# Performance work log

Hardware: AMD Instinct MI355X
Metric: run time of the kernel (lower is better)

The kernel has to match this reference:

```python
import jax, jax.numpy as jnp
import numpy as np

B, LAT, H, D, T = 2048, 32, 256, 20, 512  # batch, latent, hidden, output, max_len


def setup_inputs() -> dict:
    key = jax.random.key(0)
    ks = jax.random.split(key, 16)
    s = 0.05  # weight scale
    n = lambda k, shape, sc=s: jax.random.normal(k, shape, dtype=jnp.float32) * sc
    return {
        "z": n(ks[0], (B, LAT), 1.0),
        "target_lengths": jax.random.randint(ks[1], (B,), 1, T + 1),
        "max_len": T,
        # latent -> initial hidden / cell (hidden_dim * num_layers outputs)
        "w_lh": n(ks[2], (2 * H, LAT)), "b_lh": n(ks[3], (2 * H,)),
        "w_lc": n(ks[4], (2 * H, LAT)), "b_lc": n(ks[5], (2 * H,)),
        # LSTM layer 0 (input = output_dim), gates ordered i,f,g,o (PyTorch)
        "w_ih0": n(ks[6], (4 * H, D)), "w_hh0": n(ks[7], (4 * H, H)),
        "b_ih0": n(ks[8], (4 * H,)), "b_hh0": n(ks[9], (4 * H,)),
        # LSTM layer 1 (input = hidden_dim)
        "w_ih1": n(ks[10], (4 * H, H)), "w_hh1": n(ks[11], (4 * H, H)),
        "b_ih1": n(ks[12], (4 * H,)), "b_hh1": n(ks[13], (4 * H,)),
        # output projection
        "w_proj": n(ks[14], (D, H)), "b_proj": n(ks[15], (D,)),
    }


def _lstm_cell(x, h, c, w_ih, w_hh, b_ih, b_hh):
    g = x @ w_ih.T + b_ih + h @ w_hh.T + b_hh  # [B, 4H]
    i, f, gg, o = jnp.split(g, 4, axis=-1)
    c = jax.nn.sigmoid(f) * c + jax.nn.sigmoid(i) * jnp.tanh(gg)
    h = jax.nn.sigmoid(o) * jnp.tanh(c)
    return h, c


def reference(z, target_lengths, max_len,
              w_lh, b_lh, w_lc, b_lc,
              w_ih0, w_hh0, b_ih0, b_hh0,
              w_ih1, w_hh1, b_ih1, b_hh1,
              w_proj, b_proj):
    batch = z.shape[0]
    hid = w_hh0.shape[1]
    out_dim = w_ih0.shape[1]
    # initial per-layer states: view(B, num_layers, H)
    h_init = (z @ w_lh.T + b_lh).reshape(batch, 2, hid)
    c_init = (z @ w_lc.T + b_lc).reshape(batch, 2, hid)
    h0, h1 = h_init[:, 0], h_init[:, 1]
    c0, c1 = c_init[:, 0], c_init[:, 1]
    x0 = jnp.zeros((batch, out_dim), dtype=z.dtype)

    def step(carry, _):
        x, h0, c0, h1, c1 = carry
        h0, c0 = _lstm_cell(x, h0, c0, w_ih0, w_hh0, b_ih0, b_hh0)
        h1, c1 = _lstm_cell(h0, h1, c1, w_ih1, w_hh1, b_ih1, b_hh1)
        y = h1 @ w_proj.T + b_proj  # [B, D], fed back as next input
        return (y, h0, c0, h1, c1), y

    _, ys = jax.lax.scan(step, (x0, h0, c0, h1, c1), None, length=int(max_len))
    return jnp.transpose(ys, (1, 0, 2))  # [B, T, D]
```

## Files before the change

kernel.cpp:

```cpp
#include <hip/hip_runtime.h>
#include <hip/hip_bf16.h>

#define NB 32
#define TT 512
#define DD 20

using bf16x8 = __attribute__((ext_vector_type(8))) short;
using f32x4  = __attribute__((ext_vector_type(4))) float;

typedef __attribute__((address_space(3))) unsigned int lds_uint;
typedef __attribute__((address_space(1))) unsigned int glob_uint;

#define OFF_WSTR  0
#define OFF_WPROJ 1638400
#define OFF_B0    1654784
#define OFF_B1    1658880
#define OFF_EXCH  1662976
#define OFF_FLAG  3760128
#define WS_NEED_QUAD 3762176
#define WQUARTER  409600
#define WSTR_BYTES 1638400

#define QM_H0    0
#define QM_H1    16896
#define QM_XB    33792
#define QM_WPS   35840
#define QM_ZB    52224
#define QM_RING  56320
#define QM_TOTAL 121856

#define SM_RING  0
#define SM_H0    98304
#define SM_H1    115200
#define SM_XB    132096
#define SM_WPS   134144
#define SM_ZB    150528
#define SM_TOTAL 154624

__device__ __forceinline__ float sigf(float x) { return 1.0f / (1.0f + __expf(-x)); }
__device__ __forceinline__ float tanhfast(float x) { return 1.0f - 2.0f / (__expf(2.0f * x) + 1.0f); }

__device__ __forceinline__ void stage16(const char* g, const char* l) {
    __builtin_amdgcn_global_load_lds((glob_uint*)g, (lds_uint*)l, 16, 0, 0);
}

#define BARRIER_LK do { \
    asm volatile("s_waitcnt lgkmcnt(0)" ::: "memory"); \
    __builtin_amdgcn_s_barrier(); \
    asm volatile("" ::: "memory"); \
    __builtin_amdgcn_sched_barrier(0); \
} while (0)

__global__ void prep_quad(const float* __restrict__ wih0, const float* __restrict__ whh0,
                          const float* __restrict__ wih1, const float* __restrict__ whh1,
                          const float* __restrict__ wproj,
                          const float* __restrict__ bih0, const float* __restrict__ bhh0,
                          const float* __restrict__ bih1, const float* __restrict__ bhh1,
                          char* __restrict__ ws) {
    int idx = blockIdx.x * 256 + threadIdx.x;
    if (idx < 819200) {
        int g  = idx / 204800;
        int r  = idx - g * 204800;
        int u  = r >> 13;
        int r2 = r & 8191;
        int w  = r2 >> 11;
        int r3 = r2 & 2047;
        int q  = r3 >> 9;
        int e2 = r3 & 511;
        const float* src; int K, kt;
        if (u < 8)       { src = whh0; K = 256; kt = u; }
        else if (u == 8) { src = wih0; K = 20;  kt = 0; }
        else if (u < 17) { src = whh1; K = 256; kt = u - 9; }
        else             { src = wih1; K = 256; kt = u - 17; }
        int NT = q * 16 + g * 4 + w;
        int j = e2 & 7, lane = e2 >> 3;
        int n = NT * 16 + (lane & 15);
        int k = kt * 32 + ((lane >> 4) << 3) + j;
        float v = (k < K) ? src[n * K + k] : 0.0f;
        ((__hip_bfloat16*)(ws + OFF_WSTR))[idx] = __float2bfloat16(v);
    } else if (idx < 827392) {
        int e = idx - 819200;
        int j = e & 7, lane = (e >> 3) & 63, tile = e >> 9;
        int kt = tile & 7, nt = tile >> 3;
        int n = nt * 16 + (lane & 15);
        int k = kt * 32 + ((lane >> 4) << 3) + j;
        float v = (n < 20) ? wproj[n * 256 + k] : 0.0f;
        ((__hip_bfloat16*)(ws + OFF_WPROJ))[e] = __float2bfloat16(v);
    } else if (idx < 828416) {
        int j = idx - 827392; ((float*)(ws + OFF_B0))[j] = bih0[j] + bhh0[j];
    } else if (idx < 829440) {
        int j = idx - 828416; ((float*)(ws + OFF_B1))[j] = bih1[j] + bhh1[j];
    } else if (idx < 829952) {
        ((unsigned int*)(ws + OFF_FLAG))[idx - 829440] = 0;
    }
}

__global__ __launch_bounds__(256, 1) void decoder_quad(
    const float* __restrict__ z, const float* __restrict__ w_lh, const float* __restrict__ b_lh,
    const float* __restrict__ w_lc, const float* __restrict__ b_lc,
    const float* __restrict__ b_proj, char* __restrict__ ws,
    float* __restrict__ out) {

    __shared__ __align__(16) char smem[QM_TOTAL];

    const int tid = threadIdx.x;
    const int grp = blockIdx.x & 63;
    const int g   = blockIdx.x >> 6;
    const int b0  = grp * NB;

    __hip_bfloat16* h0p = (__hip_bfloat16*)(smem + QM_H0);
    __hip_bfloat16* h1p = (__hip_bfloat16*)(smem + QM_H1);
    __hip_bfloat16* xbh = (__hip_bfloat16*)(smem + QM_XB);

    {
        float* zbf = (float*)(smem + QM_ZB);
        #pragma unroll
        for (int i = 0; i < 4; i++) {
            int ii = tid + i * 256;
            zbf[ii] = z[(b0 + (ii >> 5)) * 32 + (ii & 31)];
        }
        ((unsigned int*)(smem + QM_XB))[tid]       = 0;
        ((unsigned int*)(smem + QM_XB))[tid + 256] = 0;
        const bf16x8* sp = (const bf16x8*)(ws + OFF_WPROJ);
        bf16x8* dp = (bf16x8*)(smem + QM_WPS);
        #pragma unroll
        for (int i = 0; i < 4; i++) dp[tid + i * 256] = sp[tid + i * 256];
    }
    __syncthreads();

    {
        float* cinitf = (float*)(smem + QM_RING);
        const float* zbf = (const float*)(smem + QM_ZB);
        for (int ii = 0; ii < 64; ii++) {
            int pi = ii * 256 + tid;
            int b = pi >> 9, col = pi & 511;
            float dh = b_lh[col], dc = b_lc[col];
            #pragma unroll 8
            for (int k = 0; k < 32; k++) {
                float zv = zbf[b * 32 + k];
                dh += zv * w_lh[col * 32 + k];
                dc += zv * w_lc[col * 32 + k];
            }
            if (col < 256) { h0p[b * 264 + col]         = __float2bfloat16(dh); cinitf[b * 256 + col]                 = dc; }
            else           { h1p[b * 264 + (col - 256)] = __float2bfloat16(dh); cinitf[8192 + b * 256 + (col - 256)] = dc; }
        }
    }
    __syncthreads();

    const int w  = tid >> 6, ln = tid & 63;
    const int l15 = ln & 15, lq = ln >> 4;
    const int lnoff = ln * 16;
    const int colg = g * 64 + w * 16 + l15;

    float c0r[2][4], c1r[2][4];
    {
        const float* cinitf = (const float*)(smem + QM_RING);
        #pragma unroll
        for (int mt = 0; mt < 2; mt++)
            #pragma unroll
            for (int r = 0; r < 4; r++) {
                int m = mt * 16 + lq * 4 + r;
                c0r[mt][r] = cinitf[m * 256 + colg];
                c1r[mt][r] = cinitf[8192 + m * 256 + colg];
            }
    }
    __syncthreads();

    const float* bias0 = (const float*)(ws + OFF_B0);
    const float* bias1 = (const float*)(ws + OFF_B1);
    float bs0[4], bs1[4];
    #pragma unroll
    for (int q = 0; q < 4; q++) {
        bs0[q] = bias0[q * 256 + colg];
        bs1[q] = bias1[q * 256 + colg];
    }
    const int pc_nt = w & 1, pc_mt = w >> 1;
    const int pc_col = pc_nt * 16 + l15;
    const float bpj = (pc_col < 20) ? b_proj[pc_col] : 0.0f;

    const char* wps_c = smem + QM_WPS;
    const char* h0c = smem + QM_H0;
    const char* h1c = smem + QM_H1;
    const char* xbc = smem + QM_XB;
    float* outp = out;

    const char* wgl   = ws + OFF_WSTR + g * WQUARTER + w * 4096 + lnoff;
    char*       ringb = smem + QM_RING + w * 16384;
    const char* ringc = smem + QM_RING + w * 16384 + lnoff;
    int sOff = 0;
    int slS  = 0;
    int slR  = 0;

    f32x4 acc[4][2];
    bf16x8 wT0, wT1, wT2, wT3, afA, afB;

#define STAGE_NEXT do { \
    stage16(wgl + sOff,        ringb + slS * 4096); \
    stage16(wgl + sOff + 1024, ringb + slS * 4096 + 1024); \
    stage16(wgl + sOff + 2048, ringb + slS * 4096 + 2048); \
    stage16(wgl + sOff + 3072, ringb + slS * 4096 + 3072); \
    sOff += 16384; if (sOff >= WQUARTER) sOff = 0; \
    slS = (slS + 1) & 3; \
} while (0)

#define WWAIT do { \
    asm volatile("s_waitcnt vmcnt(8)" ::: "memory"); \
    __builtin_amdgcn_sched_barrier(0); \
} while (0)

#define LOADW do { \
    const char* rb_ = ringc + slR * 4096; slR = (slR + 1) & 3; \
    wT0 = *(const bf16x8*)(rb_); \
    wT1 = *(const bf16x8*)(rb_ + 1024); \
    wT2 = *(const bf16x8*)(rb_ + 2048); \
    wT3 = *(const bf16x8*)(rb_ + 3072); \
} while (0)

#define LOADA(hsrc, ktv) do { \
    afA = *(const bf16x8*)((hsrc) + l15 * 528 + (ktv) * 64 + lq * 16); \
    afB = *(const bf16x8*)((hsrc) + (16 + l15) * 528 + (ktv) * 64 + lq * 16); \
} while (0)

#define LOADAX do { \
    afA = *(const bf16x8*)(xbc + l15 * 64 + lq * 16); \
    afB = *(const bf16x8*)(xbc + (16 + l15) * 64 + lq * 16); \
} while (0)

#define MFMA8 do { \
    acc[0][0] = __builtin_amdgcn_mfma_f32_16x16x32_bf16(afA, wT0, acc[0][0], 0, 0, 0); \
    acc[0][1] = __builtin_amdgcn_mfma_f32_16x16x32_bf16(afB, wT0, acc[0][1], 0, 0, 0); \
    acc[1][0] = __builtin_amdgcn_mfma_f32_16x16x32_bf16(afA, wT1, acc[1][0], 0, 0, 0); \
    acc[1][1] = __builtin_amdgcn_mfma_f32_16x16x32_bf16(afB, wT1, acc[1][1], 0, 0, 0); \
    acc[2][0] = __builtin_amdgcn_mfma_f32_16x16x32_bf16(afA, wT2, acc[2][0], 0, 0, 0); \
    acc[2][1] = __builtin_amdgcn_mfma_f32_16x16x32_bf16(afB, wT2, acc[2][1], 0, 0, 0); \
    acc[3][0] = __builtin_amdgcn_mfma_f32_16x16x32_bf16(afA, wT3, acc[3][0], 0, 0, 0); \
    acc[3][1] = __builtin_amdgcn_mfma_f32_16x16x32_bf16(afB, wT3, acc[3][1], 0, 0, 0); \
} while (0)

    auto phaseC = [&](int t) {
        f32x4 py = {bpj, bpj, bpj, bpj};
        #pragma unroll
        for (int kt = 0; kt < 8; kt++) {
            bf16x8 ah = *(const bf16x8*)(h1c + (pc_mt * 16 + l15) * 528 + kt * 64 + lq * 16);
            bf16x8 wf = *(const bf16x8*)(wps_c + pc_nt * 8192 + kt * 1024 + lnoff);
            py = __builtin_amdgcn_mfma_f32_16x16x32_bf16(ah, wf, py, 0, 0, 0);
        }
        if (pc_col < 20) {
            #pragma unroll
            for (int r = 0; r < 4; r++) {
                int row = pc_mt * 16 + lq * 4 + r;
                if (g == 0)
                    outp[((size_t)(b0 + row) * TT + (t - 1)) * DD + pc_col] = py[r];
                xbh[row * 32 + pc_col] = __float2bfloat16(py[r]);
            }
        }
    };

    unsigned int* exBase = (unsigned int*)(ws + OFF_EXCH);
    unsigned int* flBase = (unsigned int*)(ws + OFF_FLAG);

    auto exchStore = [&](int L, const char* hp, int t) {
        unsigned int* exO = exBase + ((grp * 2 + L) * 4 + g) * 1024;
        unsigned int* flO = flBase + (grp * 2 + L) * 4 + g;
        #pragma unroll
        for (int i = 0; i < 4; i++) {
            int wi = tid * 4 + i, m = wi >> 5, cp = wi & 31;
            unsigned int v = *(const unsigned int*)(hp + m * 528 + g * 128 + cp * 4);
            __hip_atomic_store(&exO[wi], v, __ATOMIC_RELAXED, __HIP_MEMORY_SCOPE_AGENT);
        }
        asm volatile("s_waitcnt vmcnt(0)" ::: "memory");
        if (tid == 0)
            __hip_atomic_store(flO, (unsigned int)(t + 1), __ATOMIC_RELAXED, __HIP_MEMORY_SCOPE_AGENT);
    };

    auto exchFinish = [&](int L, char* hp, unsigned int expect) {
        if (tid < 3) {
            int p = tid + (tid >= g);
            unsigned int* flP = flBase + (grp * 2 + L) * 4 + p;
            int spins = 0;
            while (__hip_atomic_load(flP, __ATOMIC_RELAXED, __HIP_MEMORY_SCOPE_AGENT) < expect) {
                __builtin_amdgcn_s_sleep(8);
                if (++spins > (1 << 11)) break;
            }
        }
        BARRIER_LK;
        #pragma unroll
        for (int pp = 0; pp < 3; pp++) {
            int p = pp + (pp >= g);
            unsigned int* exP = exBase + ((grp * 2 + L) * 4 + p) * 1024;
            unsigned int pv[4];
            #pragma unroll
            for (int i = 0; i < 4; i++)
                pv[i] = __hip_atomic_load(&exP[tid * 4 + i], __ATOMIC_RELAXED, __HIP_MEMORY_SCOPE_AGENT);
            #pragma unroll
            for (int i = 0; i < 4; i++) {
                int wi = tid * 4 + i, m = wi >> 5, cp = wi & 31;
                *(unsigned int*)(hp + m * 528 + p * 128 + cp * 4) = pv[i];
            }
        }
        BARRIER_LK;
    };

    STAGE_NEXT;
    STAGE_NEXT;
    STAGE_NEXT;
    WWAIT;
    LOADW;
    LOADA(h0c, 0);

    #pragma unroll 1
    for (int t = 0; t < TT; t++) {
        #pragma unroll
        for (int q = 0; q < 4; q++) {
            f32x4 v = {bs0[q], bs0[q], bs0[q], bs0[q]};
            acc[q][0] = v; acc[q][1] = v;
        }
        #pragma unroll 1
        for (int kt = 0; kt < 7; kt++) {
            STAGE_NEXT; MFMA8; WWAIT; LOADW; LOADA(h0c, kt + 1);
        }
        if (t > 0) {
            exchFinish(1, (char*)(smem + QM_H1), (unsigned int)t);
            phaseC(t);
        }
        BARRIER_LK;
        STAGE_NEXT; MFMA8; WWAIT; LOADW; LOADAX;
        STAGE_NEXT; MFMA8; WWAIT; LOADW; LOADA(h1c, 0);
        BARRIER_LK;

        #pragma unroll
        for (int mt = 0; mt < 2; mt++)
            #pragma unroll
            for (int r = 0; r < 4; r++) {
                float iv = acc[0][mt][r], fv = acc[1][mt][r];
                float gv = acc[2][mt][r], ov = acc[3][mt][r];
                float cn = sigf(fv) * c0r[mt][r] + sigf(iv) * tanhfast(gv);
                float hn = sigf(ov) * tanhfast(cn);
                c0r[mt][r] = cn;
                h0p[(mt * 16 + lq * 4 + r) * 264 + colg] = __float2bfloat16(hn);
            }
        BARRIER_LK;
        exchStore(0, h0c, t);

        #pragma unroll
        for (int q = 0; q < 4; q++) {
            f32x4 v = {bs1[q], bs1[q], bs1[q], bs1[q]};
            acc[q][0] = v; acc[q][1] = v;
        }
        #pragma unroll 1
        for (int kt = 0; kt < 7; kt++) {
            STAGE_NEXT; MFMA8; WWAIT; LOADW; LOADA(h1c, kt + 1);
        }
        STAGE_NEXT; MFMA8; WWAIT; LOADW;
        exchFinish(0, (char*)(smem + QM_H0), (unsigned int)(t + 1));
        LOADA(h0c, 0);
        #pragma unroll 1
        for (int kt = 0; kt < 7; kt++) {
            STAGE_NEXT; MFMA8; WWAIT; LOADW; LOADA(h0c, kt + 1);
        }
        STAGE_NEXT; MFMA8; WWAIT; LOADW; LOADA(h0c, 0);
        BARRIER_LK;

        #pragma unroll
        for (int mt = 0; mt < 2; mt++)
            #pragma unroll
            for (int r = 0; r < 4; r++) {
                float iv = acc[0][mt][r], fv = acc[1][mt][r];
                float gv = acc[2][mt][r], ov = acc[3][mt][r];
                float cn = sigf(fv) * c1r[mt][r] + sigf(iv) * tanhfast(gv);
                float hn = sigf(ov) * tanhfast(cn);
                c1r[mt][r] = cn;
                h1p[(mt * 16 + lq * 4 + r) * 264 + colg] = __float2bfloat16(hn);
            }
        BARRIER_LK;
        exchStore(1, h1c, t);
    }

    exchFinish(1, (char*)(smem + QM_H1), (unsigned int)TT);
    phaseC(TT);

#undef STAGE_NEXT
#undef WWAIT
#undef LOADW
#undef LOADA
#undef LOADAX
#undef MFMA8
}


__global__ void prep_solo(const float* __restrict__ wih0, const float* __restrict__ whh0,
                          const float* __restrict__ wih1, const float* __restrict__ whh1,
                          const float* __restrict__ wproj,
                          const float* __restrict__ bih0, const float* __restrict__ bhh0,
                          const float* __restrict__ bih1, const float* __restrict__ bhh1,
                          char* __restrict__ ws) {
    int idx = blockIdx.x * 256 + threadIdx.x;
    if (idx < 819200) {
        int s  = idx >> 12;
        int wv = (idx >> 9) & 7;
        int e2 = idx & 511;
        int u = s >> 2, qq = s & 3, half = u & 1;
        const float* src; int K, kt;
        if (u < 16)      { src = whh0; K = 256; kt = u >> 1; }
        else if (u < 18) { src = wih0; K = 20;  kt = 0; }
        else if (u < 34) { src = wih1; K = 256; kt = (u - 18) >> 1; }
        else             { src = whh1; K = 256; kt = (u - 34) >> 1; }
        int NT = half * 32 + (qq >> 1) * 16 + wv * 2 + (qq & 1);
        int j = e2 & 7, lane = e2 >> 3;
        int n = NT * 16 + (lane & 15);
        int k = kt * 32 + ((lane >> 4) << 3) + j;
        float v = (k < K) ? src[n * K + k] : 0.0f;
        ((__hip_bfloat16*)(ws + OFF_WSTR))[idx] = __float2bfloat16(v);
    } else if (idx < 827392) {
        int e = idx - 819200;
        int j = e & 7, lane = (e >> 3) & 63, tile = e >> 9;
        int kt = tile & 7, nt = tile >> 3;
        int n = nt * 16 + (lane & 15);
        int k = kt * 32 + ((lane >> 4) << 3) + j;
        float v = (n < 20) ? wproj[n * 256 + k] : 0.0f;
        ((__hip_bfloat16*)(ws + OFF_WPROJ))[e] = __float2bfloat16(v);
    } else if (idx < 828416) {
        int j = idx - 827392; ((float*)(ws + OFF_B0))[j] = bih0[j] + bhh0[j];
    } else if (idx < 829440) {
        int j = idx - 828416; ((float*)(ws + OFF_B1))[j] = bih1[j] + bhh1[j];
    }
}

__global__ __launch_bounds__(512, 1) void decoder_solo(
    const float* __restrict__ z, const float* __restrict__ w_lh, const float* __restrict__ b_lh,
    const float* __restrict__ w_lc, const float* __restrict__ b_lc,
    const float* __restrict__ b_proj, const char* __restrict__ ws,
    float* __restrict__ out) {

    __shared__ __align__(16) char smem[SM_TOTAL];

    const int tid = threadIdx.x;
    const int b0  = blockIdx.x * NB;

    __hip_bfloat16* h0p = (__hip_bfloat16*)(smem + SM_H0);
    __hip_bfloat16* h1p = (__hip_bfloat16*)(smem + SM_H1);
    __hip_bfloat16* xbh = (__hip_bfloat16*)(smem + SM_XB);

    {
        float* zbf = (float*)(smem + SM_ZB);
        zbf[tid]       = z[(b0 + (tid >> 5)) * 32 + (tid & 31)];
        int i2 = tid + 512;
        zbf[i2]        = z[(b0 + (i2 >> 5)) * 32 + (i2 & 31)];
        ((unsigned int*)(smem + SM_XB))[tid] = 0;
        const bf16x8* sp = (const bf16x8*)(ws + OFF_WPROJ);
        bf16x8* dp = (bf16x8*)(smem + SM_WPS);
        dp[tid] = sp[tid];
        dp[tid + 512] = sp[tid + 512];
    }
    __syncthreads();

    {
        float* cinitf = (float*)smem;
        const float* zbf = (const float*)(smem + SM_ZB);
        for (int ii = 0; ii < 32; ii++) {
            int pi = ii * 512 + tid;
            int b = pi >> 9, col = pi & 511;
            float dh = b_lh[col], dc = b_lc[col];
            #pragma unroll 8
            for (int k = 0; k < 32; k++) {
                float zv = zbf[b * 32 + k];
                dh += zv * w_lh[col * 32 + k];
                dc += zv * w_lc[col * 32 + k];
            }
            if (col < 256) { h0p[b * 264 + col]         = __float2bfloat16(dh); cinitf[b * 256 + col]                 = dc; }
            else           { h1p[b * 264 + (col - 256)] = __float2bfloat16(dh); cinitf[8192 + b * 256 + (col - 256)] = dc; }
        }
    }
    __syncthreads();

    const int wv = tid >> 6, ln = tid & 63;
    const int l15 = ln & 15, lq = ln >> 4;
    const int lnoff = ln * 16;

    float c0r[2][2][4], c1r[2][2][4];
    {
        const float* cinitf = (const float*)smem;
        #pragma unroll
        for (int mt = 0; mt < 2; mt++)
            #pragma unroll
            for (int h = 0; h < 2; h++)
                #pragma unroll
                for (int r = 0; r < 4; r++) {
                    int m = mt * 16 + lq * 4 + r, u = wv * 32 + h * 16 + l15;
                    c0r[mt][h][r] = cinitf[m * 256 + u];
                    c1r[mt][h][r] = cinitf[8192 + m * 256 + u];
                }
    }
    __syncthreads();

    const float* bias0 = (const float*)(ws + OFF_B0);
    const float* bias1 = (const float*)(ws + OFF_B1);
    float bs0[8], bs1[8];
    #pragma unroll
    for (int q = 0; q < 8; q++) {
        int col = (q >> 1) * 256 + wv * 32 + (q & 1) * 16 + l15;
        bs0[q] = bias0[col];
        bs1[q] = bias1[col];
    }
    const int pc_nt = wv & 1, pc_mt = wv >> 1;
    const int pc_col = pc_nt * 16 + l15;
    const float bpj = (wv < 4 && pc_col < 20) ? b_proj[pc_col] : 0.0f;

    const char* wps_c = smem + SM_WPS;
    const char* h0c = smem + SM_H0;
    const char* h1c = smem + SM_H1;
    const char* xbc = smem + SM_XB;

    float* outp = out;

    const char* wgl   = ws + OFF_WSTR + wv * 1024 + lnoff;
    char*       ringb = smem + SM_RING + wv * 12288;
    const char* ringc = smem + SM_RING + wv * 12288 + lnoff;
    int sOff = 2 * 32768;
    int slS  = 2;
    int slR  = 0;

    f32x4 acc[8][2];

    auto doPanel = [&](const char* hsrc, int kt, bool isX, int qbase) {
        bf16x8 af0, af1;
        if (isX) {
            af0 = *(const bf16x8*)(xbc + l15 * 64 + lq * 16);
            af1 = *(const bf16x8*)(xbc + (16 + l15) * 64 + lq * 16);
        } else {
            af0 = *(const bf16x8*)(hsrc + l15 * 528 + kt * 64 + lq * 16);
            af1 = *(const bf16x8*)(hsrc + (16 + l15) * 528 + kt * 64 + lq * 16);
        }
        #pragma unroll
        for (int j = 0; j < 4; j++)
            stage16(wgl + (sOff + j * 8192), ringb + slS * 4096 + j * 1024);
        sOff += 32768; if (sOff >= WSTR_BYTES) sOff = 0;
        slS = (slS == 2) ? 0 : slS + 1;
        asm volatile("s_waitcnt vmcnt(8)" ::: "memory");
        __builtin_amdgcn_sched_barrier(0);
        const char* rb = ringc + slR * 4096;
        slR = (slR == 2) ? 0 : slR + 1;
        bf16x8 w0 = *(const bf16x8*)(rb);
        bf16x8 w1 = *(const bf16x8*)(rb + 1024);
        bf16x8 w2 = *(const bf16x8*)(rb + 2048);
        bf16x8 w3 = *(const bf16x8*)(rb + 3072);
        acc[qbase + 0][0] = __builtin_amdgcn_mfma_f32_16x16x32_bf16(af0, w0, acc[qbase + 0][0], 0, 0, 0);
        acc[qbase + 0][1] = __builtin_amdgcn_mfma_f32_16x16x32_bf16(af1, w0, acc[qbase + 0][1], 0, 0, 0);
        acc[qbase + 1][0] = __builtin_amdgcn_mfma_f32_16x16x32_bf16(af0, w1, acc[qbase + 1][0], 0, 0, 0);
        acc[qbase + 1][1] = __builtin_amdgcn_mfma_f32_16x16x32_bf16(af1, w1, acc[qbase + 1][1], 0, 0, 0);
        acc[qbase + 2][0] = __builtin_amdgcn_mfma_f32_16x16x32_bf16(af0, w2, acc[qbase + 2][0], 0, 0, 0);
        acc[qbase + 2][1] = __builtin_amdgcn_mfma_f32_16x16x32_bf16(af1, w2, acc[qbase + 2][1], 0, 0, 0);
        acc[qbase + 3][0] = __builtin_amdgcn_mfma_f32_16x16x32_bf16(af0, w3, acc[qbase + 3][0], 0, 0, 0);
        acc[qbase + 3][1] = __builtin_amdgcn_mfma_f32_16x16x32_bf16(af1, w3, acc[qbase + 3][1], 0, 0, 0);
    };

    auto phaseC = [&](int t) {
        f32x4 py = {bpj, bpj, bpj, bpj};
        #pragma unroll
        for (int kt = 0; kt < 8; kt++) {
            bf16x8 ah = *(const bf16x8*)(h1c + (pc_mt * 16 + l15) * 528 + kt * 64 + lq * 16);
            bf16x8 wf = *(const bf16x8*)(wps_c + pc_nt * 8192 + kt * 1024 + lnoff);
            py = __builtin_amdgcn_mfma_f32_16x16x32_bf16(ah, wf, py, 0, 0, 0);
        }
        if (pc_col < 20) {
            #pragma unroll
            for (int r = 0; r < 4; r++) {
                int row = pc_mt * 16 + lq * 4 + r;
                outp[((size_t)(b0 + row) * TT + (t - 1)) * DD + pc_col] = py[r];
                xbh[row * 32 + pc_col] = __float2bfloat16(py[r]);
            }
        }
    };

    #pragma unroll
    for (int j = 0; j < 4; j++) stage16(wgl + j * 8192,         ringb + j * 1024);
    #pragma unroll
    for (int j = 0; j < 4; j++) stage16(wgl + 32768 + j * 8192, ringb + 4096 + j * 1024);

    #pragma unroll 1
    for (int t = 0; t < TT; t++) {
        #pragma unroll
        for (int q = 0; q < 8; q++) {
            f32x4 v = {bs0[q], bs0[q], bs0[q], bs0[q]};
            acc[q][0] = v; acc[q][1] = v;
        }
        if (t > 0 && wv < 4) phaseC(t);
        #pragma unroll 1
        for (int uu = 0; uu < 7; uu++) {
            doPanel(h0c, uu, false, 0);
            doPanel(h0c, uu, false, 4);
        }
        BARRIER_LK;
        doPanel(h0c, 7, false, 0);
        doPanel(h0c, 7, false, 4);
        doPanel(xbc, 0, true,  0);
        doPanel(xbc, 0, true,  4);
        BARRIER_LK;

        #pragma unroll
        for (int mt = 0; mt < 2; mt++)
            #pragma unroll
            for (int h = 0; h < 2; h++)
                #pragma unroll
                for (int r = 0; r < 4; r++) {
                    float iv = acc[0 + h][mt][r], fv = acc[2 + h][mt][r];
                    float gv = acc[4 + h][mt][r], ov = acc[6 + h][mt][r];
                    float cn = sigf(fv) * c0r[mt][h][r] + sigf(iv) * tanhfast(gv);
                    float hn = sigf(ov) * tanhfast(cn);
                    c0r[mt][h][r] = cn;
                    h0p[(mt * 16 + lq * 4 + r) * 264 + wv * 32 + h * 16 + l15] = __float2bfloat16(hn);
                }
        BARRIER_LK;

        #pragma unroll
        for (int q = 0; q < 8; q++) {
            f32x4 v = {bs1[q], bs1[q], bs1[q], bs1[q]};
            acc[q][0] = v; acc[q][1] = v;
        }
        #pragma unroll 1
        for (int uu = 0; uu < 8; uu++) {
            doPanel(h0c, uu, false, 0);
            doPanel(h0c, uu, false, 4);
        }
        #pragma unroll 1
        for (int uu = 0; uu < 8; uu++) {
            doPanel(h1c, uu, false, 0);
            doPanel(h1c, uu, false, 4);
        }
        BARRIER_LK;

        #pragma unroll
        for (int mt = 0; mt < 2; mt++)
            #pragma unroll
            for (int h = 0; h < 2; h++)
                #pragma unroll
                for (int r = 0; r < 4; r++) {
                    float iv = acc[0 + h][mt][r], fv = acc[2 + h][mt][r];
                    float gv = acc[4 + h][mt][r], ov = acc[6 + h][mt][r];
                    float cn = sigf(fv) * c1r[mt][h][r] + sigf(iv) * tanhfast(gv);
                    float hn = sigf(ov) * tanhfast(cn);
                    c1r[mt][h][r] = cn;
                    h1p[(mt * 16 + lq * 4 + r) * 264 + wv * 32 + h * 16 + l15] = __float2bfloat16(hn);
                }
        BARRIER_LK;
    }

    if (wv < 4) phaseC(TT);
}


extern "C" void kernel_launch(void* const* d_in, const int* in_sizes, int n_in,
                              void* d_out, int out_size, void* d_ws, size_t ws_size,
                              hipStream_t stream) {
    const float* z      = (const float*)d_in[0];
    const float* w_lh   = (const float*)d_in[3];
    const float* b_lh   = (const float*)d_in[4];
    const float* w_lc   = (const float*)d_in[5];
    const float* b_lc   = (const float*)d_in[6];
    const float* w_ih0  = (const float*)d_in[7];
    const float* w_hh0  = (const float*)d_in[8];
    const float* b_ih0  = (const float*)d_in[9];
    const float* b_hh0  = (const float*)d_in[10];
    const float* w_ih1  = (const float*)d_in[11];
    const float* w_hh1  = (const float*)d_in[12];
    const float* b_ih1  = (const float*)d_in[13];
    const float* b_hh1  = (const float*)d_in[14];
    const float* w_proj = (const float*)d_in[15];
    const float* b_proj = (const float*)d_in[16];
    char* ws = (char*)d_ws;
    float* out = (float*)d_out;

    if (ws_size >= (size_t)WS_NEED_QUAD) {
        prep_quad<<<3242, 256, 0, stream>>>(w_ih0, w_hh0, w_ih1, w_hh1, w_proj,
                                            b_ih0, b_hh0, b_ih1, b_hh1, ws);
        decoder_quad<<<256, 256, 0, stream>>>(z, w_lh, b_lh, w_lc, b_lc, b_proj, ws, out);
    } else {
        prep_solo<<<3240, 256, 0, stream>>>(w_ih0, w_hh0, w_ih1, w_hh1, w_proj,
                                            b_ih0, b_hh0, b_ih1, b_hh1, ws);
        decoder_solo<<<64, 512, 0, stream>>>(z, w_lh, b_lh, w_lc, b_lc, b_proj, ws, out);
    }
}
```

Baseline: 6.163 ms.

## Split K-dimension of LSTM gate GEMMs across eight waves with LDS reduction

Doubles the block to 512 threads so two wave groups split the K tiles of each gate GEMM (even vs odd tiles), with the upper waves writing partial accumulators to a new LDS reduction buffer that the lower waves add before the gate nonlinearity. The weight staging ring becomes a per-wave double buffer with statically scheduled unit indices, and the output projection moves to the upper waves. The intent is to cut the serial per-step MFMA chain latency in the recurrent loop, at the cost of extra LDS traffic, more barriers, and higher LDS usage.

```diff
diff --git a/kernel.cpp b/kernel.cpp
--- a/kernel.cpp
+++ b/kernel.cpp
@@ -26,8 +26,9 @@
 #define QM_XB    33792
 #define QM_WPS   35840
 #define QM_ZB    52224
-#define QM_RING  56320
-#define QM_TOTAL 121856
+#define QM_RED   56320
+#define QM_RING  90112
+#define QM_TOTAL 155648
 
 #define SM_RING  0
 #define SM_H0    98304
@@ -95,7 +96,7 @@
     }
 }
 
-__global__ __launch_bounds__(256, 1) void decoder_quad(
+__global__ __launch_bounds__(512, 1) void decoder_quad8(
     const float* __restrict__ z, const float* __restrict__ w_lh, const float* __restrict__ b_lh,
     const float* __restrict__ w_lc, const float* __restrict__ b_lc,
     const float* __restrict__ b_proj, char* __restrict__ ws,
@@ -114,25 +115,22 @@
 
     {
         float* zbf = (float*)(smem + QM_ZB);
-        #pragma unroll
-        for (int i = 0; i < 4; i++) {
-            int ii = tid + i * 256;
-            zbf[ii] = z[(b0 + (ii >> 5)) * 32 + (ii & 31)];
-        }
-        ((unsigned int*)(smem + QM_XB))[tid]       = 0;
-        ((unsigned int*)(smem + QM_XB))[tid + 256] = 0;
+        zbf[tid]       = z[(b0 + (tid >> 5)) * 32 + (tid & 31)];
+        int i2 = tid + 512;
+        zbf[i2]        = z[(b0 + (i2 >> 5)) * 32 + (i2 & 31)];
+        ((unsigned int*)(smem + QM_XB))[tid] = 0;
         const bf16x8* sp = (const bf16x8*)(ws + OFF_WPROJ);
         bf16x8* dp = (bf16x8*)(smem + QM_WPS);
-        #pragma unroll
-        for (int i = 0; i < 4; i++) dp[tid + i * 256] = sp[tid + i * 256];
+        dp[tid] = sp[tid];
+        dp[tid + 512] = sp[tid + 512];
     }
     __syncthreads();
 
     {
-        float* cinitf = (float*)(smem + QM_RING);
+        float* cinitf = (float*)(smem + QM_RED);
         const float* zbf = (const float*)(smem + QM_ZB);
-        for (int ii = 0; ii < 64; ii++) {
-            int pi = ii * 256 + tid;
+        for (int ii = 0; ii < 32; ii++) {
+            int pi = ii * 512 + tid;
             int b = pi >> 9, col = pi & 511;
             float dh = b_lh[col], dc = b_lc[col];
             #pragma unroll 8
@@ -147,14 +145,15 @@
     }
     __syncthreads();
 
-    const int w  = tid >> 6, ln = tid & 63;
+    const int w   = tid >> 6, ln = tid & 63;
+    const int wlo = w & 3;
     const int l15 = ln & 15, lq = ln >> 4;
     const int lnoff = ln * 16;
-    const int colg = g * 64 + w * 16 + l15;
+    const int colg = g * 64 + wlo * 16 + l15;
 
     float c0r[2][4], c1r[2][4];
-    {
-        const float* cinitf = (const float*)(smem + QM_RING);
+    if (w < 4) {
+        const float* cinitf = (const float*)(smem + QM_RED);
         #pragma unroll
         for (int mt = 0; mt < 2; mt++)
             #pragma unroll
@@ -174,9 +173,9 @@
         bs0[q] = bias0[q * 256 + colg];
         bs1[q] = bias1[q * 256 + colg];
     }
-    const int pc_nt = w & 1, pc_mt = w >> 1;
+    const int pc_nt = wlo & 1, pc_mt = wlo >> 1;
     const int pc_col = pc_nt * 16 + l15;
-    const float bpj = (pc_col < 20) ? b_proj[pc_col] : 0.0f;
+    const float bpj = (w >= 4 && pc_col < 20) ? b_proj[pc_col] : 0.0f;
 
     const char* wps_c = smem + QM_WPS;
     const char* h0c = smem + QM_H0;
@@ -184,32 +183,31 @@
     const char* xbc = smem + QM_XB;
     float* outp = out;
 
-    const char* wgl   = ws + OFF_WSTR + g * WQUARTER + w * 4096 + lnoff;
-    char*       ringb = smem + QM_RING + w * 16384;
-    const char* ringc = smem + QM_RING + w * 16384 + lnoff;
-    int sOff = 0;
-    int slS  = 0;
-    int slR  = 0;
+    const char* wgl   = ws + OFF_WSTR + g * WQUARTER + wlo * 4096 + lnoff;
+    char*       ringb = smem + QM_RING + w * 8192;
+    const char* ringc = smem + QM_RING + w * 8192 + lnoff;
+    int slS = 0, slR = 0;
 
     f32x4 acc[4][2];
     bf16x8 wT0, wT1, wT2, wT3, afA, afB;
 
-#define STAGE_NEXT do { \
-    stage16(wgl + sOff,        ringb + slS * 4096); \
-    stage16(wgl + sOff + 1024, ringb + slS * 4096 + 1024); \
-    stage16(wgl + sOff + 2048, ringb + slS * 4096 + 2048); \
-    stage16(wgl + sOff + 3072, ringb + slS * 4096 + 3072); \
-    sOff += 16384; if (sOff >= WQUARTER) sOff = 0; \
-    slS = (slS + 1) & 3; \
+#define STAGE_U(u) do { \
+    const char* gs_ = wgl + (u) * 16384; \
+    char* ld_ = ringb + slS * 4096; \
+    stage16(gs_,        ld_); \
+    stage16(gs_ + 1024, ld_ + 1024); \
+    stage16(gs_ + 2048, ld_ + 2048); \
+    stage16(gs_ + 3072, ld_ + 3072); \
+    slS ^= 1; \
 } while (0)
 
 #define WWAIT do { \
-    asm volatile("s_waitcnt vmcnt(8)" ::: "memory"); \
+    asm volatile("s_waitcnt vmcnt(4)" ::: "memory"); \
     __builtin_amdgcn_sched_barrier(0); \
 } while (0)
 
 #define LOADW do { \
-    const char* rb_ = ringc + slR * 4096; slR = (slR + 1) & 3; \
+    const char* rb_ = ringc + slR * 4096; slR ^= 1; \
     wT0 = *(const bf16x8*)(rb_); \
     wT1 = *(const bf16x8*)(rb_ + 1024); \
     wT2 = *(const bf16x8*)(rb_ + 2048); \
@@ -237,6 +235,38 @@
     acc[3][1] = __builtin_amdgcn_mfma_f32_16x16x32_bf16(afB, wT3, acc[3][1], 0, 0, 0); \
 } while (0)
 
+#define DOP(hsrc, ktv, uNext) do { \
+    WWAIT; LOADW; LOADA(hsrc, ktv); MFMA8; \
+    __builtin_amdgcn_sched_barrier(0); \
+    STAGE_U(uNext); \
+} while (0)
+
+#define DOPX(uNext) do { \
+    WWAIT; LOADW; LOADAX; MFMA8; \
+    __builtin_amdgcn_sched_barrier(0); \
+    STAGE_U(uNext); \
+} while (0)
+
+#define ACC_SET(b_) do { _Pragma("unroll") for (int q = 0; q < 4; q++) { \
+    f32x4 v_ = {(b_)[q], (b_)[q], (b_)[q], (b_)[q]}; acc[q][0] = v_; acc[q][1] = v_; } } while (0)
+#define ACC_ZERO do { _Pragma("unroll") for (int q = 0; q < 4; q++) { \
+    f32x4 v_ = {0.f, 0.f, 0.f, 0.f}; acc[q][0] = v_; acc[q][1] = v_; } } while (0)
+
+    char* redme = smem + QM_RED + wlo * 8448 + ln * 132;
+
+    auto redWrite = [&]() {
+        #pragma unroll
+        for (int c = 0; c < 8; c++)
+            *(f32x4*)(redme + c * 16) = acc[c >> 1][c & 1];
+    };
+    auto redAdd = [&]() {
+        #pragma unroll
+        for (int c = 0; c < 8; c++) {
+            f32x4 pv = *(const f32x4*)(redme + c * 16);
+            acc[c >> 1][c & 1] += pv;
+        }
+    };
+
     auto phaseC = [&](int t) {
         f32x4 py = {bpj, bpj, bpj, bpj};
         #pragma unroll
@@ -260,17 +290,19 @@
     unsigned int* flBase = (unsigned int*)(ws + OFF_FLAG);
 
     auto exchStore = [&](int L, const char* hp, int t) {
-        unsigned int* exO = exBase + ((grp * 2 + L) * 4 + g) * 1024;
-        unsigned int* flO = flBase + (grp * 2 + L) * 4 + g;
-        #pragma unroll
-        for (int i = 0; i < 4; i++) {
-            int wi = tid * 4 + i, m = wi >> 5, cp = wi & 31;
-            unsigned int v = *(const unsigned int*)(hp + m * 528 + g * 128 + cp * 4);
-            __hip_atomic_store(&exO[wi], v, __ATOMIC_RELAXED, __HIP_MEMORY_SCOPE_AGENT);
-        }
-        asm volatile("s_waitcnt vmcnt(0)" ::: "memory");
-        if (tid == 0)
-            __hip_atomic_store(flO, (unsigned int)(t + 1), __ATOMIC_RELAXED, __HIP_MEMORY_SCOPE_AGENT);
+        if (w < 4) {
+            unsigned int* exO = exBase + ((grp * 2 + L) * 4 + g) * 1024;
+            unsigned int* flO = flBase + (grp * 2 + L) * 4 + g;
+            #pragma unroll
+            for (int i = 0; i < 4; i++) {
+                int wi = tid * 4 + i, m = wi >> 5, cp = wi & 31;
+                unsigned int v = *(const unsigned int*)(hp + m * 528 + g * 128 + cp * 4);
+                __hip_atomic_store(&exO[wi], v, __ATOMIC_RELAXED, __HIP_MEMORY_SCOPE_AGENT);
+            }
+            asm volatile("s_waitcnt vmcnt(0)" ::: "memory");
+            if (tid == 0)
+                __hip_atomic_store(flO, (unsigned int)(t + 1), __ATOMIC_RELAXED, __HIP_MEMORY_SCOPE_AGENT);
+        }
     };
 
     auto exchFinish = [&](int L, char* hp, unsigned int expect) {
@@ -288,103 +320,109 @@
         for (int pp = 0; pp < 3; pp++) {
             int p = pp + (pp >= g);
             unsigned int* exP = exBase + ((grp * 2 + L) * 4 + p) * 1024;
-            unsigned int pv[4];
-            #pragma unroll
-            for (int i = 0; i < 4; i++)
-                pv[i] = __hip_atomic_load(&exP[tid * 4 + i], __ATOMIC_RELAXED, __HIP_MEMORY_SCOPE_AGENT);
-            #pragma unroll
-            for (int i = 0; i < 4; i++) {
-                int wi = tid * 4 + i, m = wi >> 5, cp = wi & 31;
+            unsigned int pv[2];
+            #pragma unroll
+            for (int i = 0; i < 2; i++)
+                pv[i] = __hip_atomic_load(&exP[tid * 2 + i], __ATOMIC_RELAXED, __HIP_MEMORY_SCOPE_AGENT);
+            #pragma unroll
+            for (int i = 0; i < 2; i++) {
+                int wi = tid * 2 + i, m = wi >> 5, cp = wi & 31;
                 *(unsigned int*)(hp + m * 528 + p * 128 + cp * 4) = pv[i];
             }
         }
         BARRIER_LK;
     };
 
-    STAGE_NEXT;
-    STAGE_NEXT;
-    STAGE_NEXT;
-    WWAIT;
-    LOADW;
-    LOADA(h0c, 0);
+    if (w < 4) { STAGE_U(0); STAGE_U(2); }
+    else       { STAGE_U(1); STAGE_U(3); }
 
     #pragma unroll 1
     for (int t = 0; t < TT; t++) {
-        #pragma unroll
-        for (int q = 0; q < 4; q++) {
-            f32x4 v = {bs0[q], bs0[q], bs0[q], bs0[q]};
-            acc[q][0] = v; acc[q][1] = v;
-        }
-        #pragma unroll 1
-        for (int kt = 0; kt < 7; kt++) {
-            STAGE_NEXT; MFMA8; WWAIT; LOADW; LOADA(h0c, kt + 1);
+        if (w < 4) {
+            ACC_SET(bs0);
+            DOP(h0c, 0, 4); DOP(h0c, 2, 6); DOP(h0c, 4, 8); DOP(h0c, 6, 9);
+        } else {
+            ACC_ZERO;
+            DOP(h0c, 1, 5); DOP(h0c, 3, 7); DOP(h0c, 5, 10); DOP(h0c, 7, 12);
         }
         if (t > 0) {
             exchFinish(1, (char*)(smem + QM_H1), (unsigned int)t);
-            phaseC(t);
-        }
-        BARRIER_LK;
-        STAGE_NEXT; MFMA8; WWAIT; LOADW; LOADAX;
-        STAGE_NEXT; MFMA8; WWAIT; LOADW; LOADA(h1c, 0);
-        BARRIER_LK;
-
-        #pragma unroll
-        for (int mt = 0; mt < 2; mt++)
-            #pragma unroll
-            for (int r = 0; r < 4; r++) {
-                float iv = acc[0][mt][r], fv = acc[1][mt][r];
-                float gv = acc[2][mt][r], ov = acc[3][mt][r];
-                float cn = sigf(fv) * c0r[mt][r] + sigf(iv) * tanhfast(gv);
-                float hn = sigf(ov) * tanhfast(cn);
-                c0r[mt][r] = cn;
-                h0p[(mt * 16 + lq * 4 + r) * 264 + colg] = __float2bfloat16(hn);
-            }
+            if (w >= 4) phaseC(t);
+        }
+        BARRIER_LK;
+        if (w < 4) {
+            DOPX(11);
+        } else {
+            redWrite();
+            ACC_ZERO;
+            DOP(h1c, 1, 14);
+        }
+        BARRIER_LK;
+        if (w < 4) {
+            redAdd();
+            #pragma unroll
+            for (int mt = 0; mt < 2; mt++)
+                #pragma unroll
+                for (int r = 0; r < 4; r++) {
+                    float iv = acc[0][mt][r], fv = acc[1][mt][r];
+                    float gv = acc[2][mt][r], ov = acc[3][mt][r];
+                    float cn = sigf(fv) * c0r[mt][r] + sigf(iv) * tanhfast(gv);
+                    float hn = sigf(ov) * tanhfast(cn);
+                    c0r[mt][r] = cn;
+                    h0p[(mt * 16 + lq * 4 + r) * 264 + colg] = __float2bfloat16(hn);
+                }
+            ACC_SET(bs1);
+        } else {
+            DOP(h1c, 3, 16);
+        }
         BARRIER_LK;
         exchStore(0, h0c, t);
 
-        #pragma unroll
-        for (int q = 0; q < 4; q++) {
-            f32x4 v = {bs1[q], bs1[q], bs1[q], bs1[q]};
-            acc[q][0] = v; acc[q][1] = v;
-        }
-        #pragma unroll 1
-        for (int kt = 0; kt < 7; kt++) {
-            STAGE_NEXT; MFMA8; WWAIT; LOADW; LOADA(h1c, kt + 1);
-        }
-        STAGE_NEXT; MFMA8; WWAIT; LOADW;
+        if (w < 4) {
+            DOP(h1c, 0, 13); DOP(h1c, 2, 15); DOP(h1c, 4, 17); DOP(h1c, 6, 19);
+        } else {
+            DOP(h1c, 5, 18); DOP(h1c, 7, 20);
+        }
         exchFinish(0, (char*)(smem + QM_H0), (unsigned int)(t + 1));
-        LOADA(h0c, 0);
-        #pragma unroll 1
-        for (int kt = 0; kt < 7; kt++) {
-            STAGE_NEXT; MFMA8; WWAIT; LOADW; LOADA(h0c, kt + 1);
-        }
-        STAGE_NEXT; MFMA8; WWAIT; LOADW; LOADA(h0c, 0);
-        BARRIER_LK;
-
-        #pragma unroll
-        for (int mt = 0; mt < 2; mt++)
-            #pragma unroll
-            for (int r = 0; r < 4; r++) {
-                float iv = acc[0][mt][r], fv = acc[1][mt][r];
-                float gv = acc[2][mt][r], ov = acc[3][mt][r];
-                float cn = sigf(fv) * c1r[mt][r] + sigf(iv) * tanhfast(gv);
-                float hn = sigf(ov) * tanhfast(cn);
-                c1r[mt][r] = cn;
-                h1p[(mt * 16 + lq * 4 + r) * 264 + colg] = __float2bfloat16(hn);
-            }
+
+        if (w < 4) {
+            DOP(h0c, 0, 21); DOP(h0c, 2, 23); DOP(h0c, 4, 0); DOP(h0c, 6, 2);
+        } else {
+            DOP(h0c, 1, 22); DOP(h0c, 3, 24); DOP(h0c, 5, 1); DOP(h0c, 7, 3);
+            redWrite();
+        }
+        BARRIER_LK;
+        if (w < 4) {
+            redAdd();
+            #pragma unroll
+            for (int mt = 0; mt < 2; mt++)
+                #pragma unroll
+                for (int r = 0; r < 4; r++) {
+                    float iv = acc[0][mt][r], fv = acc[1][mt][r];
+                    float gv = acc[2][mt][r], ov = acc[3][mt][r];
+                    float cn = sigf(fv) * c1r[mt][r] + sigf(iv) * tanhfast(gv);
+                    float hn = sigf(ov) * tanhfast(cn);
+                    c1r[mt][r] = cn;
+                    h1p[(mt * 16 + lq * 4 + r) * 264 + colg] = __float2bfloat16(hn);
+                }
+        }
         BARRIER_LK;
         exchStore(1, h1c, t);
     }
 
     exchFinish(1, (char*)(smem + QM_H1), (unsigned int)TT);
-    phaseC(TT);
-
-#undef STAGE_NEXT
+    if (w >= 4) phaseC(TT);
+
+#undef STAGE_U
 #undef WWAIT
 #undef LOADW
 #undef LOADA
 #undef LOADAX
 #undef MFMA8
+#undef DOP
+#undef DOPX
+#undef ACC_SET
+#undef ACC_ZERO
 }
 
 
@@ -673,7 +711,7 @@
     if (ws_size >= (size_t)WS_NEED_QUAD) {
         prep_quad<<<3242, 256, 0, stream>>>(w_ih0, w_hh0, w_ih1, w_hh1, w_proj,
                                             b_ih0, b_hh0, b_ih1, b_hh1, ws);
-        decoder_quad<<<256, 256, 0, stream>>>(z, w_lh, b_lh, w_lc, b_lc, b_proj, ws, out);
+        decoder_quad8<<<256, 512, 0, stream>>>(z, w_lh, b_lh, w_lc, b_lc, b_proj, ws, out);
     } else {
         prep_solo<<<3240, 256, 0, stream>>>(w_ih0, w_hh0, w_ih1, w_hh1, w_proj,
                                             b_ih0, b_hh0, b_ih1, b_hh1, ws);
```

New measurement: 11.33 ms. 1.84x slower.
